# Performance work log

Hardware: AMD Instinct MI355X
Metric: run time of the kernel (lower is better)

The kernel has to match this reference:

```python
import jax, jax.numpy as jnp
import numpy as np

N_NODES = 16000
N_EDGES = 128000
IN_FEAT = 1024   # nb_iprs
OUT_FEAT = 1024  # RelGraphConv out / embed_dim
N_RELS = 7
NB_GOS = 4096


def setup_inputs() -> dict:
    key = jax.random.key(0)
    ks = jax.random.split(key, 9)
    feat = jax.random.normal(ks[0], (N_NODES, IN_FEAT), dtype=jnp.float32)
    src = jax.random.randint(ks[1], (N_EDGES,), 0, N_NODES, dtype=jnp.int32)
    dst = jax.random.randint(ks[2], (N_EDGES,), 0, N_NODES, dtype=jnp.int32)
    etypes = jax.random.randint(ks[3], (N_EDGES,), 0, N_RELS, dtype=jnp.int32)
    # RelGraphConv params (regularizer=None): per-relation weight, self-loop weight, bias
    s = 1.0 / np.sqrt(IN_FEAT)
    W_rel = jax.random.uniform(ks[4], (N_RELS, IN_FEAT, OUT_FEAT), dtype=jnp.float32, minval=-s, maxval=s)
    W_loop = jax.random.uniform(ks[5], (IN_FEAT, OUT_FEAT), dtype=jnp.float32, minval=-s, maxval=s)
    bias = jnp.zeros((OUT_FEAT,), dtype=jnp.float32)
    # GO embeddings, init U(-k, k) with k = sqrt(1/embed_dim)
    k = 1.0 / np.sqrt(OUT_FEAT)
    go_embed = jax.random.uniform(ks[6], (NB_GOS, OUT_FEAT), dtype=jnp.float32, minval=-k, maxval=k)
    go_rad = jax.random.uniform(ks[7], (NB_GOS, 1), dtype=jnp.float32, minval=-k, maxval=k)
    return {"feat": feat, "src": src, "dst": dst, "etypes": etypes,
            "W_rel": W_rel, "W_loop": W_loop, "bias": bias,
            "go_embed": go_embed, "go_rad": go_rad}


def reference(feat, src, dst, etypes, W_rel, W_loop, bias, go_embed, go_rad):
    n = feat.shape[0]
    # RelGraphConv (sum aggregation, self-loop, bias, no activation):
    # message on edge e: feat[src[e]] @ W_rel[etypes[e]]; by linearity, first
    # segment-sum source features per (dst, rel), then one batched GEMM.
    x_src = feat[src]                                   # [E, in]
    seg = dst.astype(jnp.int32) * N_RELS + etypes       # combined (dst, rel) id
    agg = jax.ops.segment_sum(x_src, seg, num_segments=n * N_RELS)
    agg = agg.reshape(n, N_RELS, IN_FEAT)               # [N, R, in]
    h = jnp.einsum('nri,rio->no', agg, W_rel) + feat @ W_loop + bias  # [N, out]
    # scoring: sigmoid(x @ E_go^T + |rad|)
    logits = jax.nn.sigmoid(h @ go_embed.T + jnp.abs(go_rad).reshape(1, -1))
    return logits
```

## Files before the change

### kernel.cpp

```cpp
#include <hip/hip_runtime.h>
#include <math.h>

#define N_NODES 16000
#define N_EDGES 128000
#define KDIM 1024
#define N_RELS 7
#define NB_GOS 4096
#define KCAT (KDIM * (N_RELS + 1))
#define MPAD 16128

#define BM 128
#define BN 128
#define BK 32
#define CAP2 (N_EDGES + N_RELS * BM)
#define NTILE_E (CAP2 / BM)

typedef __attribute__((ext_vector_type(8))) short bf16x8;
typedef __attribute__((ext_vector_type(8))) unsigned short u16x8;
typedef __attribute__((ext_vector_type(4))) float f32x4;

__device__ __forceinline__ unsigned short f2bf(float f) {
    union { float f; unsigned int u; } v; v.f = f;
    unsigned int u = v.u + 0x7FFFu + ((v.u >> 16) & 1u);
    return (unsigned short)(u >> 16);
}

__device__ __forceinline__ void gload16(const void* g, void* lds) {
    __builtin_amdgcn_global_load_lds(
        (const __attribute__((address_space(1))) unsigned int*)g,
        (__attribute__((address_space(3))) unsigned int*)lds, 16, 0, 0);
}


__global__ __launch_bounds__(256) void conv_bf16(const float* __restrict__ in,
                                                 unsigned short* __restrict__ out, int n8) {
    int i = blockIdx.x * 256 + threadIdx.x;
    if (i >= n8) return;
    const float4* in4 = (const float4*)in;
    float4 x = in4[2 * i], y = in4[2 * i + 1];
    u16x8 o;
    o[0] = f2bf(x.x); o[1] = f2bf(x.y); o[2] = f2bf(x.z); o[3] = f2bf(x.w);
    o[4] = f2bf(y.x); o[5] = f2bf(y.y); o[6] = f2bf(y.z); o[7] = f2bf(y.w);
    *(u16x8*)&out[(size_t)i * 8] = o;
}

__global__ __launch_bounds__(256) void conv_cat(const float* __restrict__ in,
                                                unsigned short* __restrict__ Acat) {
    int i = blockIdx.x * 256 + threadIdx.x;
    if (i >= N_NODES * (KDIM / 8)) return;
    int n = i >> 7, c8 = (i & 127) * 8;
    const float4* in4 = (const float4*)(in + (size_t)n * KDIM + c8);
    float4 x = in4[0], y = in4[1];
    u16x8 o;
    o[0] = f2bf(x.x); o[1] = f2bf(x.y); o[2] = f2bf(x.z); o[3] = f2bf(x.w);
    o[4] = f2bf(y.x); o[5] = f2bf(y.y); o[6] = f2bf(y.z); o[7] = f2bf(y.w);
    *(u16x8*)&Acat[(size_t)n * KCAT + c8] = o;
}

__global__ void transpose_w(const float* __restrict__ Wrel,
                            const float* __restrict__ Wloop,
                            unsigned short* __restrict__ WrelT,
                            unsigned short* __restrict__ WloopT) {
    __shared__ float t[32][33];
    int z = blockIdx.z;
    const float* src = (z < N_RELS) ? Wrel + (size_t)z * KDIM * KDIM : Wloop;
    unsigned short* dst = (z < N_RELS) ? WrelT + (size_t)z * KDIM * KDIM : WloopT;
    int tx = threadIdx.x, ty = threadIdx.y;
    int x = blockIdx.x * 32 + tx;
    int y0 = blockIdx.y * 32;
    #pragma unroll
    for (int j = 0; j < 4; j++)
        t[ty + 8 * j][tx] = src[(size_t)(y0 + ty + 8 * j) * KDIM + x];
    __syncthreads();
    #pragma unroll
    for (int j = 0; j < 4; j++) {
        int n = blockIdx.x * 32 + ty + 8 * j;
        dst[(size_t)n * KDIM + y0 + tx] = f2bf(t[tx][ty + 8 * j]);
    }
}

__global__ void transpose_cat(const float* __restrict__ Wrel,
                              const float* __restrict__ Wloop,
                              unsigned short* __restrict__ BT) {
    __shared__ float t[32][33];
    int z = blockIdx.z;
    const float* src = (z == 0) ? Wloop : Wrel + (size_t)(z - 1) * KDIM * KDIM;
    int tx = threadIdx.x, ty = threadIdx.y;
    int x = blockIdx.x * 32 + tx;
    int y0 = blockIdx.y * 32;
    #pragma unroll
    for (int j = 0; j < 4; j++)
        t[ty + 8 * j][tx] = src[(size_t)(y0 + ty + 8 * j) * KDIM + x];
    __syncthreads();
    #pragma unroll
    for (int j = 0; j < 4; j++) {
        int o = blockIdx.x * 32 + ty + 8 * j;
        BT[(size_t)o * KCAT + z * KDIM + y0 + tx] = f2bf(t[tx][ty + 8 * j]);
    }
}


__global__ void zero_ints(int* p, int n) {
    int i = blockIdx.x * 256 + threadIdx.x;
    if (i < n) p[i] = 0;
}

__global__ void hist_dst(const int* __restrict__ dst, int* cnt) {
    int e = blockIdx.x * 256 + threadIdx.x;
    if (e < N_EDGES) atomicAdd(&cnt[dst[e]], 1);
}

__global__ __launch_bounds__(1024) void scan_offs(const int* __restrict__ cnt,
                                                  int* __restrict__ offs) {
    __shared__ int part[1024];
    int t = threadIdx.x;
    int base = t * 16;
    int local[16];
    int s = 0;
    if (base < N_NODES) {
        #pragma unroll
        for (int j = 0; j < 16; j++) { local[j] = cnt[base + j]; s += local[j]; }
    }
    part[t] = s;
    __syncthreads();
    for (int d = 1; d < 1024; d <<= 1) {
        int v = (t >= d) ? part[t - d] : 0;
        __syncthreads();
        part[t] += v;
        __syncthreads();
    }
    if (base < N_NODES) {
        int ex = (t == 0) ? 0 : part[t - 1];
        #pragma unroll
        for (int j = 0; j < 16; j++) { offs[base + j] = ex; ex += local[j]; }
        if (base + 16 == N_NODES) offs[N_NODES] = ex;
    }
}

__global__ void scatter_dst(const int* __restrict__ src, const int* __restrict__ dst,
                            const int* __restrict__ et, const int* __restrict__ offs,
                            int* cursor, int* __restrict__ se) {
    int e = blockIdx.x * 256 + threadIdx.x;
    if (e < N_EDGES) {
        int d = dst[e];
        int p = atomicAdd(&cursor[d], 1);
        se[offs[d] + p] = (src[e] << 3) | et[e];
    }
}

__global__ __launch_bounds__(256) void aggregate(const float* __restrict__ feat,
                                                 const int* __restrict__ offs,
                                                 const int* __restrict__ se,
                                                 unsigned short* __restrict__ Acat) {
    int n = blockIdx.x;
    int t = threadIdx.x;
    int e0 = offs[n], e1 = offs[n + 1];
    float4 a0 = {0,0,0,0}, a1 = a0, a2 = a0, a3 = a0, a4 = a0, a5 = a0, a6 = a0;
    const float4* f4 = (const float4*)feat;
    for (int i = e0; i < e1; i++) {
        int v = se[i];
        int s = v >> 3, r = v & 7;
        float4 x = f4[(size_t)s * (KDIM / 4) + t];
        #define ADD4(a) { a.x += x.x; a.y += x.y; a.z += x.z; a.w += x.w; }
        switch (r) {
            case 0: ADD4(a0) break; case 1: ADD4(a1) break;
            case 2: ADD4(a2) break; case 3: ADD4(a3) break;
            case 4: ADD4(a4) break; case 5: ADD4(a5) break;
            default: ADD4(a6) break;
        }
        #undef ADD4
    }
    unsigned short* row = Acat + (size_t)n * KCAT + KDIM;
    #define ST4(rr, a) { ushort4 o; o.x = f2bf(a.x); o.y = f2bf(a.y); \
                         o.z = f2bf(a.z); o.w = f2bf(a.w); \
                         *(ushort4*)(row + rr * KDIM + t * 4) = o; }
    ST4(0, a0) ST4(1, a1) ST4(2, a2) ST4(3, a3) ST4(4, a4) ST4(5, a5) ST4(6, a6)
    #undef ST4
}


template<int MODE, int KD>
__global__ __launch_bounds__(512, 2) void gemm256(
    const unsigned short* __restrict__ A,
    const unsigned short* __restrict__ BT,
    const float* __restrict__ br,
    void* __restrict__ outv)
{
    __shared__ unsigned short As[2][256 * 64];
    __shared__ unsigned short Bs[2][256 * 64];

    const int tid = threadIdx.x;
    const int l = tid & 63, w = tid >> 6;
    const int wm = w >> 2, wn = w & 3;
    const int lrow = l & 15, lhi = l >> 4, lx = l & 7;

    const int nwg = gridDim.x * gridDim.y;
    const int b = blockIdx.y * gridDim.x + blockIdx.x;
    const int q8 = nwg >> 3, r8 = nwg & 7;
    const int xcd = b & 7, idx = b >> 3;
    const int wg = (xcd < r8 ? xcd * (q8 + 1) : r8 * (q8 + 1) + (xcd - r8) * q8) + idx;
    const int m0 = (wg % gridDim.y) * 256;
    const int n0 = (wg / gridDim.y) * 256;

    const int NI = (KD >> 6) >> 1;

    const int rr = tid >> 3;
    const int cc = (tid & 7) ^ (rr & 7);

    const unsigned short* gA = A + (size_t)(m0 + rr) * KD + cc * 8;
    const unsigned short* gB = BT + (size_t)(n0 + (rr & 31) + (rr >> 5) * 64) * KD + cc * 8;

    auto stageA = [&](int dbuf, int kt, int half) {
        #pragma unroll
        for (int j = 0; j < 2; j++)
            gload16(gA + (size_t)(j * 128 + half * 64) * KD + kt * 64,
                    &As[dbuf][(size_t)(w * 8 + j * 128 + half * 64) * 64]);
    };
    auto stageB = [&](int dbuf, int kt, int half) {
        #pragma unroll
        for (int j = 0; j < 2; j++)
            gload16(gB + (size_t)(j * 128 + half * 32) * KD + kt * 64,
                    &Bs[dbuf][(size_t)((w & 3) * 8 + (w >> 2) * 64 + j * 128 + half * 32) * 64]);
    };

    stageA(0, 0, 0); stageB(0, 0, 0); stageA(0, 0, 1); stageB(0, 0, 1);
    stageA(1, 1, 0); stageB(1, 1, 0);
    asm volatile("s_waitcnt vmcnt(4)" ::: "memory");
    __builtin_amdgcn_s_barrier();

    f32x4 acc[8][4] = {};
    bf16x8 afr[4][2], b0[2][2], b1[2][2];

#define LDA(BUF, MH) do { _Pragma("unroll")                                   \
    for (int mi = 0; mi < 4; mi++) { _Pragma("unroll")                        \
        for (int ks = 0; ks < 2; ks++) {                                      \
            const int row_ = wm * 128 + (MH) * 64 + mi * 16 + lrow;           \
            const int ch_ = (ks * 4 + lhi) ^ lx;                              \
            afr[mi][ks] = *(const bf16x8*)&As[BUF][row_ * 64 + ch_ * 8];      \
        } } } while (0)

#define LDB(BUF, NH, DST) do { _Pragma("unroll")                              \
    for (int nj = 0; nj < 2; nj++) { _Pragma("unroll")                        \
        for (int ks = 0; ks < 2; ks++) {                                      \
            const int row_ = wn * 64 + (NH) * 32 + nj * 16 + lrow;            \
            const int ch_ = (ks * 4 + lhi) ^ lx;                              \
            DST[nj][ks] = *(const bf16x8*)&Bs[BUF][row_ * 64 + ch_ * 8];      \
        } } } while (0)

#define MM2(MH) do {                                                          \
    __builtin_amdgcn_s_barrier();                                             \
    __builtin_amdgcn_s_setprio(1);                                            \
    _Pragma("unroll")                                                         \
    for (int mi = 0; mi < 4; mi++) { _Pragma("unroll")                        \
        for (int nj = 0; nj < 2; nj++) { _Pragma("unroll")                    \
            for (int ks = 0; ks < 2; ks++) {                                  \
                acc[(MH)*4+mi][nj] = __builtin_amdgcn_mfma_f32_16x16x32_bf16( \
                    afr[mi][ks], b0[nj][ks], acc[(MH)*4+mi][nj], 0, 0, 0);    \
                acc[(MH)*4+mi][2+nj] = __builtin_amdgcn_mfma_f32_16x16x32_bf16( \
                    afr[mi][ks], b1[nj][ks], acc[(MH)*4+mi][2+nj], 0, 0, 0);  \
        } } }                                                                 \
    __builtin_amdgcn_s_setprio(0); } while (0)

    for (int t = 0; t < NI; t++) {
        const bool nl = (t + 1 < NI);
        LDA(0, 0); LDB(0, 0, b0); LDB(0, 1, b1);
        stageA(1, 2 * t + 1, 1); stageB(1, 2 * t + 1, 1);
        MM2(0);
        __builtin_amdgcn_s_barrier();
        LDA(0, 1);
        if (nl) { stageA(0, 2 * t + 2, 0); stageB(0, 2 * t + 2, 0); }
        MM2(1);
        if (nl) asm volatile("s_waitcnt vmcnt(4)" ::: "memory");
        else    asm volatile("s_waitcnt vmcnt(0)" ::: "memory");
        __builtin_amdgcn_s_barrier();
        LDA(1, 0); LDB(1, 0, b0); LDB(1, 1, b1);
        if (nl) { stageA(0, 2 * t + 2, 1); stageB(0, 2 * t + 2, 1); }
        MM2(0);
        __builtin_amdgcn_s_barrier();
        LDA(1, 1);
        if (nl) { stageA(1, 2 * t + 3, 0); stageB(1, 2 * t + 3, 0); }
        MM2(1);
        if (nl) asm volatile("s_waitcnt vmcnt(4)" ::: "memory");
        else    asm volatile("s_waitcnt vmcnt(0)" ::: "memory");
        __builtin_amdgcn_s_barrier();
    }
#undef LDA
#undef LDB
#undef MM2

    const int cl = l & 15, rh = (l >> 4) * 4;
    float brv[4];
    #pragma unroll
    for (int nj = 0; nj < 4; nj++) brv[nj] = br[n0 + wn * 64 + nj * 16 + cl];
    #pragma unroll
    for (int mi = 0; mi < 8; mi++) {
        #pragma unroll
        for (int r4 = 0; r4 < 4; r4++) {
            const int row = m0 + wm * 128 + mi * 16 + rh + r4;
            if (MODE == 2 && row >= N_NODES) continue;
            #pragma unroll
            for (int nj = 0; nj < 4; nj++) {
                const int col = n0 + wn * 64 + nj * 16 + cl;
                float x = acc[mi][nj][r4];
                if (MODE == 0) {
                    ((unsigned short*)outv)[(size_t)row * KDIM + col] = f2bf(x + brv[nj]);
                } else {
                    x += fabsf(brv[nj]);
                    ((float*)outv)[(size_t)row * (size_t)NB_GOS + col] =
                        1.0f / (1.0f + __expf(-x));
                }
            }
        }
    }
}


__global__ void init_buckets(int* cnt, int* cursor, int* bucket) {
    int i = blockIdx.x * 256 + threadIdx.x;
    if (i < 8) { cnt[i] = 0; cursor[i] = 0; }
    if (i < CAP2) bucket[i] = -1;
}

__global__ __launch_bounds__(256) void count_etypes(const int* __restrict__ et, int* cnt) {
    __shared__ int lc[N_RELS];
    if (threadIdx.x < N_RELS) lc[threadIdx.x] = 0;
    __syncthreads();
    int e = blockIdx.x * 256 + threadIdx.x;
    if (e < N_EDGES) atomicAdd(&lc[et[e]], 1);
    __syncthreads();
    if (threadIdx.x < N_RELS) atomicAdd(&cnt[threadIdx.x], lc[threadIdx.x]);
}

__global__ void calc_offsets(const int* __restrict__ cnt, int* offs) {
    if (blockIdx.x == 0 && threadIdx.x == 0) {
        int acc = 0;
        offs[0] = 0;
        for (int r = 0; r < N_RELS; r++) {
            acc += ((cnt[r] + BM - 1) / BM) * BM;
            offs[r + 1] = acc;
        }
    }
}

__global__ __launch_bounds__(256) void scatter_edges(const int* __restrict__ et,
                                                     const int* __restrict__ offs,
                                                     int* cursor, int* bucket) {
    __shared__ int lc[N_RELS];
    __shared__ int lbase[N_RELS];
    if (threadIdx.x < N_RELS) lc[threadIdx.x] = 0;
    __syncthreads();
    int e = blockIdx.x * 256 + threadIdx.x;
    int r = 0, my = 0;
    bool valid = (e < N_EDGES);
    if (valid) { r = et[e]; my = atomicAdd(&lc[r], 1); }
    __syncthreads();
    if (threadIdx.x < N_RELS)
        lbase[threadIdx.x] = atomicAdd(&cursor[threadIdx.x], lc[threadIdx.x]);
    __syncthreads();
    if (valid) bucket[offs[r] + lbase[r] + my] = e;
}

template<int MODE>
__global__ __launch_bounds__(256) void mfma_gemm(
    const unsigned short* __restrict__ A,
    const unsigned short* __restrict__ BT,
    const float* __restrict__ br,
    float* __restrict__ out,
    const int* __restrict__ src,
    const int* __restrict__ dst,
    const int* __restrict__ bucket,
    const int* __restrict__ offs,
    int kd)
{
    __shared__ unsigned short As[BM * BK];
    __shared__ unsigned short Bs[BN * BK];
    __shared__ int s_src[BM];
    __shared__ int s_dst[BM];

    const int tid = threadIdx.x;
    const int l = tid & 63;
    const int w = tid >> 6;
    const int wr = w >> 1, wc = w & 1;

    const int nwg = gridDim.x * gridDim.y;
    const int b = blockIdx.y * gridDim.x + blockIdx.x;
    const int cpx = nwg >> 3;
    const int swz = (b & 7) * cpx + (b >> 3);
    const int n0 = (swz / gridDim.y) * BN;
    const int m0 = (swz % gridDim.y) * BM;

    const unsigned short* Bb = BT;
    if (MODE == 1) {
        int rel = -1;
        #pragma unroll
        for (int q = 0; q < N_RELS; q++)
            if (m0 >= offs[q] && m0 < offs[q + 1]) rel = q;
        if (rel < 0) return;
        Bb = BT + (size_t)rel * KDIM * KDIM;
        if (tid < BM) {
            int e = bucket[m0 + tid];
            s_src[tid] = (e >= 0) ? src[e] : -1;
            s_dst[tid] = (e >= 0) ? dst[e] : -1;
        }
        __syncthreads();
    }

    f32x4 acc[4][4] = {};

    const int s0 = tid, s1 = tid + 256;
    const int r0 = s0 >> 2, kc0 = (s0 & 3) * 8;
    const int r1 = s1 >> 2, kc1 = (s1 & 3) * 8;
    unsigned short* ldsA0 = As + (w * 64) * 8;
    unsigned short* ldsA1 = As + (w * 64 + 256) * 8;
    unsigned short* ldsB0 = Bs + (w * 64) * 8;
    unsigned short* ldsB1 = Bs + (w * 64 + 256) * 8;

    size_t arow0, arow1;
    if (MODE == 1) {
        int sr0 = s_src[r0]; arow0 = (sr0 < 0) ? 0 : (size_t)sr0;
        int sr1 = s_src[r1]; arow1 = (sr1 < 0) ? 0 : (size_t)sr1;
    } else {
        arow0 = (size_t)(m0 + r0);
        arow1 = (size_t)(m0 + r1);
    }
    const size_t brow0 = (size_t)(n0 + r0), brow1 = (size_t)(n0 + r1);

    const int fa = (wr * 64 + (l & 15)) * BK + (l >> 4) * 8;
    const int fb = (wc * 64 + (l & 15)) * BK + (l >> 4) * 8;

    for (int k0 = 0; k0 < kd; k0 += BK) {
        gload16(A + arow0 * kd + k0 + kc0, ldsA0);
        gload16(A + arow1 * kd + k0 + kc1, ldsA1);
        gload16(Bb + brow0 * kd + k0 + kc0, ldsB0);
        gload16(Bb + brow1 * kd + k0 + kc1, ldsB1);
        __syncthreads();

        bf16x8 a[4], bfr[4];
        #pragma unroll
        for (int mi = 0; mi < 4; mi++)
            a[mi] = *(const bf16x8*)&As[fa + mi * 16 * BK];
        #pragma unroll
        for (int nj = 0; nj < 4; nj++)
            bfr[nj] = *(const bf16x8*)&Bs[fb + nj * 16 * BK];
        #pragma unroll
        for (int mi = 0; mi < 4; mi++)
            #pragma unroll
            for (int nj = 0; nj < 4; nj++)
                acc[mi][nj] = __builtin_amdgcn_mfma_f32_16x16x32_bf16(a[mi], bfr[nj], acc[mi][nj], 0, 0, 0);
        __syncthreads();
    }

    const int cl = l & 15, rh = (l >> 4) * 4;
    #pragma unroll
    for (int mi = 0; mi < 4; mi++) {
        #pragma unroll
        for (int r4 = 0; r4 < 4; r4++) {
            const int row = wr * 64 + mi * 16 + rh + r4;
            if (MODE == 1) {
                const int d = s_dst[row];
                if (d >= 0) {
                    #pragma unroll
                    for (int nj = 0; nj < 4; nj++) {
                        const int col = n0 + wc * 64 + nj * 16 + cl;
                        atomicAdd(&out[(size_t)d * KDIM + col], acc[mi][nj][r4]);
                    }
                }
            } else if (MODE == 0) {
                #pragma unroll
                for (int nj = 0; nj < 4; nj++) {
                    const int col = n0 + wc * 64 + nj * 16 + cl;
                    out[(size_t)(m0 + row) * KDIM + col] = acc[mi][nj][r4] + br[col];
                }
            } else {
                #pragma unroll
                for (int nj = 0; nj < 4; nj++) {
                    const int col = n0 + wc * 64 + nj * 16 + cl;
                    float x = acc[mi][nj][r4] + fabsf(br[col]);
                    out[(size_t)(m0 + row) * (size_t)NB_GOS + col] = 1.0f / (1.0f + expf(-x));
                }
            }
        }
    }
}


extern "C" void kernel_launch(void* const* d_in, const int* in_sizes, int n_in,
                              void* d_out, int out_size, void* d_ws, size_t ws_size,
                              hipStream_t stream) {
    const float* feat   = (const float*)d_in[0];
    const int*   src    = (const int*)d_in[1];
    const int*   dst    = (const int*)d_in[2];
    const int*   etypes = (const int*)d_in[3];
    const float* W_rel  = (const float*)d_in[4];
    const float* W_loop = (const float*)d_in[5];
    const float* bias   = (const float*)d_in[6];
    const float* go_emb = (const float*)d_in[7];
    const float* go_rad = (const float*)d_in[8];
    float* out = (float*)d_out;

    const size_t ACAT_B = (size_t)MPAD * KCAT * 2;
    const size_t HB_B   = (size_t)MPAD * KDIM * 2;
    const size_t BTC_B  = (size_t)KDIM * KCAT * 2;
    const size_t GOB_B  = (size_t)NB_GOS * KDIM * 2;
    const size_t CNT_B  = 16384 * 4;
    const size_t NEED   = ACAT_B + HB_B + BTC_B + GOB_B + 3 * CNT_B + (size_t)N_EDGES * 4;

    if (ws_size >= NEED) {
        char* p = (char*)d_ws;
        unsigned short* Acat  = (unsigned short*)p;  p += ACAT_B;
        unsigned short* hb    = (unsigned short*)p;  p += HB_B;
        unsigned short* BTcat = (unsigned short*)p;  p += BTC_B;
        unsigned short* gob   = (unsigned short*)p;  p += GOB_B;
        int* cnt    = (int*)p;                       p += CNT_B;
        int* cursor = (int*)p;                       p += CNT_B;
        int* offs   = (int*)p;                       p += CNT_B;
        int* se     = (int*)p;

        zero_ints<<<(2 * 16384 + 255) / 256, 256, 0, stream>>>(cnt, 2 * 16384);
        conv_cat<<<(N_NODES * (KDIM / 8) + 255) / 256, 256, 0, stream>>>(feat, Acat);
        conv_bf16<<<(NB_GOS * KDIM / 8 + 255) / 256, 256, 0, stream>>>(go_emb, gob, NB_GOS * KDIM / 8);
        {
            dim3 g(KDIM / 32, KDIM / 32, N_RELS + 1), bb(32, 8);
            transpose_cat<<<g, bb, 0, stream>>>(W_rel, W_loop, BTcat);
        }
        hist_dst<<<(N_EDGES + 255) / 256, 256, 0, stream>>>(dst, cnt);
        scan_offs<<<1, 1024, 0, stream>>>(cnt, offs);
        scatter_dst<<<(N_EDGES + 255) / 256, 256, 0, stream>>>(src, dst, etypes, offs, cursor, se);
        aggregate<<<N_NODES, 256, 0, stream>>>(feat, offs, se, Acat);

        {
            dim3 g(KDIM / 256, MPAD / 256);
            gemm256<0, KCAT><<<g, 512, 0, stream>>>(Acat, BTcat, bias, hb);
        }
        {
            dim3 g(NB_GOS / 256, MPAD / 256);
            gemm256<2, KDIM><<<g, 512, 0, stream>>>(hb, gob, go_rad, out);
        }
        return;
    }

    char* p = (char*)d_ws;
    float* h            = (float*)p;            p += (size_t)N_NODES * KDIM * 4;
    unsigned short* fb  = (unsigned short*)p;   p += (size_t)N_NODES * KDIM * 2;
    unsigned short* wrT = (unsigned short*)p;   p += (size_t)N_RELS * KDIM * KDIM * 2;
    unsigned short* wlT = (unsigned short*)p;   p += (size_t)KDIM * KDIM * 2;
    unsigned short* gob = (unsigned short*)p;   p += (size_t)NB_GOS * KDIM * 2;
    int* cnt    = (int*)p;
    int* cursor = cnt + 8;
    int* offs   = cursor + 8;
    int* bucket = offs + 16;

    conv_bf16<<<(N_NODES * KDIM / 8 + 255) / 256, 256, 0, stream>>>(feat, fb, N_NODES * KDIM / 8);
    conv_bf16<<<(NB_GOS * KDIM / 8 + 255) / 256, 256, 0, stream>>>(go_emb, gob, NB_GOS * KDIM / 8);
    {
        dim3 g(KDIM / 32, KDIM / 32, N_RELS + 1), bb(32, 8);
        transpose_w<<<g, bb, 0, stream>>>(W_rel, W_loop, wrT, wlT);
    }
    init_buckets<<<(CAP2 + 255) / 256, 256, 0, stream>>>(cnt, cursor, bucket);
    count_etypes<<<(N_EDGES + 255) / 256, 256, 0, stream>>>(etypes, cnt);
    calc_offsets<<<1, 64, 0, stream>>>(cnt, offs);
    scatter_edges<<<(N_EDGES + 255) / 256, 256, 0, stream>>>(etypes, offs, cursor, bucket);
    {
        dim3 g(KDIM / BN, N_NODES / BM);
        mfma_gemm<0><<<g, 256, 0, stream>>>(fb, wlT, bias, h, nullptr, nullptr, nullptr, nullptr, KDIM);
    }
    {
        dim3 g(KDIM / BN, NTILE_E);
        mfma_gemm<1><<<g, 256, 0, stream>>>(fb, wrT, nullptr, h, src, dst, bucket, offs, KDIM);
    }
    conv_bf16<<<(N_NODES * KDIM / 8 + 255) / 256, 256, 0, stream>>>(h, fb, N_NODES * KDIM / 8);
    {
        dim3 g(NB_GOS / BN, N_NODES / BM);
        mfma_gemm<2><<<g, 256, 0, stream>>>(fb, gob, go_rad, out, nullptr, nullptr, nullptr, nullptr, KDIM);
    }
}
```

Before: 619.4 us.

## Double-buffer GEMM fragment registers and cut barriers in the MFMA main loop

Restructures the bf16 MFMA GEMM main loop so that A and B LDS fragments are double-buffered in registers. The next sub-tile's LDS reads are issued before the current MFMA block runs, and per-phase barriers drop from two to one. Global-to-LDS staging is regrouped and the vmcnt waits are adjusted to match. The tile-to-workgroup mapping is also changed from column-major to row-major order. The aim is to hide LDS latency and barrier stalls behind MFMA work, at the cost of more VGPRs (possible lower occupancy) and trickier wait-count correctness.

```diff
diff --git a/kernel.cpp b/kernel.cpp
--- a/kernel.cpp
+++ b/kernel.cpp
@@ -29,6 +29,12 @@
     __builtin_amdgcn_global_load_lds(
         (const __attribute__((address_space(1))) unsigned int*)g,
         (__attribute__((address_space(3))) unsigned int*)lds, 16, 0, 0);
+}
+
+__device__ __forceinline__ void bar() {
+    asm volatile("" ::: "memory");
+    __builtin_amdgcn_s_barrier();
+    asm volatile("" ::: "memory");
 }
 
 
@@ -199,8 +205,8 @@
     const int q8 = nwg >> 3, r8 = nwg & 7;
     const int xcd = b & 7, idx = b >> 3;
     const int wg = (xcd < r8 ? xcd * (q8 + 1) : r8 * (q8 + 1) + (xcd - r8) * q8) + idx;
-    const int m0 = (wg % gridDim.y) * 256;
-    const int n0 = (wg / gridDim.y) * 256;
+    const int m0 = (wg / gridDim.x) * 256;
+    const int n0 = (wg % gridDim.x) * 256;
 
     const int NI = (KD >> 6) >> 1;
 
@@ -223,20 +229,21 @@
                     &Bs[dbuf][(size_t)((w & 3) * 8 + (w >> 2) * 64 + j * 128 + half * 32) * 64]);
     };
 
-    stageA(0, 0, 0); stageB(0, 0, 0); stageA(0, 0, 1); stageB(0, 0, 1);
-    stageA(1, 1, 0); stageB(1, 1, 0);
-    asm volatile("s_waitcnt vmcnt(4)" ::: "memory");
-    __builtin_amdgcn_s_barrier();
+    stageA(0, 0, 0); stageA(0, 0, 1); stageB(0, 0, 0); stageB(0, 0, 1);
+    stageA(1, 1, 0); stageB(1, 1, 0); stageB(1, 1, 1);
+    asm volatile("s_waitcnt vmcnt(6)" ::: "memory");
+    bar();
 
     f32x4 acc[8][4] = {};
-    bf16x8 afr[4][2], b0[2][2], b1[2][2];
-
-#define LDA(BUF, MH) do { _Pragma("unroll")                                   \
+    bf16x8 afrX[4][2], afrY[4][2];
+    bf16x8 bA0[2][2], bA1[2][2], bB0[2][2], bB1[2][2];
+
+#define LDA(BUF, MH, DST) do { _Pragma("unroll")                              \
     for (int mi = 0; mi < 4; mi++) { _Pragma("unroll")                        \
         for (int ks = 0; ks < 2; ks++) {                                      \
             const int row_ = wm * 128 + (MH) * 64 + mi * 16 + lrow;           \
             const int ch_ = (ks * 4 + lhi) ^ lx;                              \
-            afr[mi][ks] = *(const bf16x8*)&As[BUF][row_ * 64 + ch_ * 8];      \
+            DST[mi][ks] = *(const bf16x8*)&As[BUF][row_ * 64 + ch_ * 8];      \
         } } } while (0)
 
 #define LDB(BUF, NH, DST) do { _Pragma("unroll")                              \
@@ -247,42 +254,44 @@
             DST[nj][ks] = *(const bf16x8*)&Bs[BUF][row_ * 64 + ch_ * 8];      \
         } } } while (0)
 
-#define MM2(MH) do {                                                          \
-    __builtin_amdgcn_s_barrier();                                             \
+#define MM2(MH, AFR, B0, B1) do {                                             \
     __builtin_amdgcn_s_setprio(1);                                            \
     _Pragma("unroll")                                                         \
     for (int mi = 0; mi < 4; mi++) { _Pragma("unroll")                        \
         for (int nj = 0; nj < 2; nj++) { _Pragma("unroll")                    \
             for (int ks = 0; ks < 2; ks++) {                                  \
                 acc[(MH)*4+mi][nj] = __builtin_amdgcn_mfma_f32_16x16x32_bf16( \
-                    afr[mi][ks], b0[nj][ks], acc[(MH)*4+mi][nj], 0, 0, 0);    \
+                    AFR[mi][ks], B0[nj][ks], acc[(MH)*4+mi][nj], 0, 0, 0);    \
                 acc[(MH)*4+mi][2+nj] = __builtin_amdgcn_mfma_f32_16x16x32_bf16( \
-                    afr[mi][ks], b1[nj][ks], acc[(MH)*4+mi][2+nj], 0, 0, 0);  \
+                    AFR[mi][ks], B1[nj][ks], acc[(MH)*4+mi][2+nj], 0, 0, 0);  \
         } } }                                                                 \
     __builtin_amdgcn_s_setprio(0); } while (0)
 
+    LDA(0, 0, afrX); LDB(0, 0, bA0); LDB(0, 1, bA1);
+
     for (int t = 0; t < NI; t++) {
         const bool nl = (t + 1 < NI);
-        LDA(0, 0); LDB(0, 0, b0); LDB(0, 1, b1);
-        stageA(1, 2 * t + 1, 1); stageB(1, 2 * t + 1, 1);
-        MM2(0);
-        __builtin_amdgcn_s_barrier();
-        LDA(0, 1);
-        if (nl) { stageA(0, 2 * t + 2, 0); stageB(0, 2 * t + 2, 0); }
-        MM2(1);
-        if (nl) asm volatile("s_waitcnt vmcnt(4)" ::: "memory");
+        LDA(0, 1, afrY);
+        stageA(1, 2 * t + 1, 1);
+        MM2(0, afrX, bA0, bA1);
+        asm volatile("s_waitcnt vmcnt(2)" ::: "memory");
+        bar();
+        LDA(1, 0, afrX); LDB(1, 0, bB0); LDB(1, 1, bB1);
+        if (nl) { stageA(0, 2 * t + 2, 0); stageB(0, 2 * t + 2, 0); stageB(0, 2 * t + 2, 1); }
+        MM2(1, afrY, bA0, bA1);
+        if (nl) asm volatile("s_waitcnt vmcnt(6)" ::: "memory");
         else    asm volatile("s_waitcnt vmcnt(0)" ::: "memory");
-        __builtin_amdgcn_s_barrier();
-        LDA(1, 0); LDB(1, 0, b0); LDB(1, 1, b1);
-        if (nl) { stageA(0, 2 * t + 2, 1); stageB(0, 2 * t + 2, 1); }
-        MM2(0);
-        __builtin_amdgcn_s_barrier();
-        LDA(1, 1);
-        if (nl) { stageA(1, 2 * t + 3, 0); stageB(1, 2 * t + 3, 0); }
-        MM2(1);
-        if (nl) asm volatile("s_waitcnt vmcnt(4)" ::: "memory");
-        else    asm volatile("s_waitcnt vmcnt(0)" ::: "memory");
-        __builtin_amdgcn_s_barrier();
+        bar();
+        LDA(1, 1, afrY);
+        if (nl) stageA(0, 2 * t + 2, 1);
+        MM2(0, afrX, bB0, bB1);
+        asm volatile("s_waitcnt vmcnt(2)" ::: "memory");
+        bar();
+        LDA(0, 0, afrX); LDB(0, 0, bA0); LDB(0, 1, bA1);
+        if (nl) { stageA(1, 2 * t + 3, 0); stageB(1, 2 * t + 3, 0); stageB(1, 2 * t + 3, 1); }
+        MM2(1, afrY, bB0, bB1);
+        if (nl) asm volatile("s_waitcnt vmcnt(6)" ::: "memory");
+        bar();
     }
 #undef LDA
 #undef LDB
```

New measurement: 1.568 ms. +153.1%, slower.
